# Kernel tuning notes

Hardware: AMD Instinct MI355X
Metric: run time of the kernel (lower is better)

## Reference

```python
import jax, jax.numpy as jnp
import numpy as np

B, N1, N2, D, H = 32, 512, 256, 256, 8
HD = D // H  # head dim = 32


def setup_inputs() -> dict:
    key = jax.random.key(0)
    ks = jax.random.split(key, 12)
    s = 0.05
    return {
        "x1": jax.random.normal(ks[0], (B, N1, D), jnp.float32),
        "x2": jax.random.normal(ks[1], (B, N2, D), jnp.float32),
        "r_w1": jax.random.normal(ks[2], (D, 2 * D), jnp.float32) * s,
        "r_b1": jnp.zeros((D,), jnp.float32),
        "ln_g": jnp.ones((D,), jnp.float32),
        "ln_b": jnp.zeros((D,), jnp.float32),
        "r_w2": jax.random.normal(ks[3], (4, D), jnp.float32) * s,
        "r_b2": jnp.zeros((4,), jnp.float32),
        "lf_w": jax.random.normal(ks[4], (D, D), jnp.float32) * s,
        "lf_b": jnp.zeros((D,), jnp.float32),
        "af2_w": jax.random.normal(ks[5], (D, D), jnp.float32) * s,
        "af2_b": jnp.zeros((D,), jnp.float32),
        "af3_w": jax.random.normal(ks[6], (N1, D), jnp.float32) * s,  # Linear(dim, num_pathway)
        "af3_b": jnp.zeros((N1,), jnp.float32),
        "attn_in_w": jax.random.normal(ks[7], (3 * D, D), jnp.float32) * s,
        "attn_in_b": jnp.zeros((3 * D,), jnp.float32),
        "attn_out_w": jax.random.normal(ks[8], (D, D), jnp.float32) * s,
        "attn_out_b": jnp.zeros((D,), jnp.float32),
    }


def _layernorm(x, g, b, eps=1e-5):
    mu = x.mean(-1, keepdims=True)
    var = ((x - mu) ** 2).mean(-1, keepdims=True)
    return (x - mu) * jax.lax.rsqrt(var + eps) * g + b


def reference(x1, x2, r_w1, r_b1, ln_g, ln_b, r_w2, r_b2,
              lf_w, lf_b, af2_w, af2_b, af3_w, af3_b,
              attn_in_w, attn_in_b, attn_out_w, attn_out_b):
    b, n1, d = x1.shape
    n2 = x2.shape[1]

    # ---- RoutingNetwork: mean-pool both modalities, small MLP, softmax ----
    m = jnp.concatenate([x1.mean(1), x2.mean(1)], axis=-1)        # [b, 2d]
    h = jax.nn.gelu(_layernorm(m @ r_w1.T + r_b1, ln_g, ln_b), approximate=False)
    logits = h @ r_w2.T + r_b2                                     # [b, 4]
    w = jax.nn.softmax(logits, axis=-1)                            # [b, 4]

    z = jnp.concatenate([x1, x2], axis=1)                          # [b, n1+n2, d]

    # ---- Expert 0: LinearFusion (dropout off at eval) ----
    lf = jax.nn.elu(z @ lf_w.T + lf_b)
    g0, i0 = lf[:, :n1, :], lf[:, n1:, :]

    # ---- Expert 1: AddFusion, n1 >= n2 branch (n2 == dim required) ----
    a1 = jax.nn.elu(x1 @ af2_w.T + af2_b)                          # [b, n1, d]
    a2 = jax.nn.elu(jnp.einsum('bnd,pn->bdp', x2, af3_w) + af3_b)  # [b, d, n1]
    a2 = a2.transpose(0, 2, 1)                                     # [b, n1, d]
    x_out = a1 + a2
    g1, i1 = x_out, x_out[:, :n2, :]

    # ---- Expert 2: AttentionFusion (MHA, 8 heads, self-attn over concat) ----
    qkv = z @ attn_in_w.T + attn_in_b                              # [b, S, 3d]
    q, k, v = jnp.split(qkv, 3, axis=-1)
    S = n1 + n2
    q = q.reshape(b, S, H, HD)
    k = k.reshape(b, S, H, HD)
    v = v.reshape(b, S, H, HD)
    scores = jnp.einsum('bqhd,bkhd->bhqk', q, k) / np.sqrt(HD)
    attn = jax.nn.softmax(scores, axis=-1)
    o = jnp.einsum('bhqk,bkhd->bqhd', attn, v).reshape(b, S, d)
    o = o @ attn_out_w.T + attn_out_b
    g2, i2 = o[:, :n1, :], o[:, n1:, :]

    # ---- Expert 3: IdentityFusion ----
    g3, i3 = x1, x2

    # ---- Soft-routing weighted combine ----
    gene_all = jnp.stack([g0, g1, g2, g3], axis=1)                 # [b, 4, n1, d]
    img_all = jnp.stack([i0, i1, i2, i3], axis=1)                  # [b, 4, n2, d]
    we = w[:, :, None, None]
    gene = (gene_all * we).sum(axis=1)
    img = (img_all * we).sum(axis=1)
    return gene, img
```

## Files before the change

### kernel.cpp

```cpp
#include <hip/hip_runtime.h>
#include <hip/hip_bf16.h>
#include <math.h>

#define B_ 32
#define N1_ 512
#define N2_ 256
#define D_ 256
#define S_ 768
#define IMG_OFF 4194304
#define QSCALE_ (0.17677669529663689f * 1.4426950408889634f)

typedef __attribute__((ext_vector_type(8))) short bf16x8;
typedef __attribute__((ext_vector_type(4))) float f32x4;
#define MFMA16(a, b, c) __builtin_amdgcn_mfma_f32_16x16x32_bf16(a, b, c, 0, 0, 0)

__device__ __forceinline__ ushort f2b(float f) {
  __hip_bfloat16 h = __float2bfloat16(f);
  return __builtin_bit_cast(ushort, h);
}
__device__ __forceinline__ uint pk2(float a, float b) {
  return (uint)f2b(a) | ((uint)f2b(b) << 16);
}
__device__ __forceinline__ float b2f(ushort u) {
  return __builtin_bit_cast(float, ((uint)u) << 16);
}
__device__ __forceinline__ float eluf(float v) { return v > 0.f ? v : expm1f(v); }

__device__ __forceinline__ void gl16(const ushort* g, ushort* l) {
  __builtin_amdgcn_global_load_lds(
      (const __attribute__((address_space(1))) uint*)g,
      (__attribute__((address_space(3))) uint*)l, 16, 0, 0);
}

__global__ __launch_bounds__(256) void k_prep(const float* __restrict__ x1,
                                              const float* __restrict__ x2,
                                              const float* __restrict__ lf_w,
                                              const float* __restrict__ af2_w,
                                              const float* __restrict__ af3_w,
                                              const float* __restrict__ attn_in_w,
                                              const float* __restrict__ attn_out_w,
                                              ushort* __restrict__ zb,
                                              ushort* __restrict__ wb,
                                              ushort* __restrict__ x2t,
                                              float* __restrict__ mp) {
  int t = threadIdx.x;
  if (blockIdx.x >= 256) {
    int g = (blockIdx.x - 256)*256 + t;
    int e0 = g*4;
    const float* src; int loc; float sc = 1.f;
    if (e0 < 65536)       { src = lf_w;       loc = e0; }
    else if (e0 < 131072) { src = af2_w;      loc = e0 - 65536; }
    else if (e0 < 262144) { src = af3_w;      loc = e0 - 131072; }
    else if (e0 < 458752) { src = attn_in_w;  loc = e0 - 262144; if (loc < 65536) sc = QSCALE_; }
    else                  { src = attn_out_w; loc = e0 - 458752; }
    float4 v = *(const float4*)(src + loc);
    *(ushort4*)(wb + e0) = make_ushort4(f2b(v.x*sc), f2b(v.y*sc), f2b(v.z*sc), f2b(v.w*sc));
    return;
  }
  int b = blockIdx.x >> 3, s = blockIdx.x & 7;
  int c = t & 63;
  int rg = t >> 6;
  __shared__ float red[4][260];
  __shared__ ushort xt[32][266];
  float4 s1 = {0.f, 0.f, 0.f, 0.f};
  for (int i = 0; i < 16; ++i) {
    int r = s*64 + rg*16 + i;
    float4 v = *(const float4*)(x1 + ((size_t)(b*N1_) + r)*D_ + c*4);
    s1.x += v.x; s1.y += v.y; s1.z += v.z; s1.w += v.w;
    uint2 pk; pk.x = pk2(v.x, v.y); pk.y = pk2(v.z, v.w);
    *(uint2*)(zb + (size_t)b*196608 + (size_t)r*256 + c*4) = pk;
  }
  red[rg][c*4+0] = s1.x; red[rg][c*4+1] = s1.y; red[rg][c*4+2] = s1.z; red[rg][c*4+3] = s1.w;
  __syncthreads();
  {
    float v = red[0][t] + red[1][t] + red[2][t] + red[3][t];
    mp[(size_t)(b*8+s)*512 + t] = v * (1.0f/512.0f);
  }
  __syncthreads();
  float4 s2 = {0.f, 0.f, 0.f, 0.f};
  for (int i = 0; i < 8; ++i) {
    int rl = rg*8 + i;
    int r = s*32 + rl;
    float4 v = *(const float4*)(x2 + ((size_t)(b*N2_) + r)*D_ + c*4);
    s2.x += v.x; s2.y += v.y; s2.z += v.z; s2.w += v.w;
    ushort b0 = f2b(v.x), b1 = f2b(v.y), b2 = f2b(v.z), b3 = f2b(v.w);
    uint2 pk; pk.x = (uint)b0 | ((uint)b1 << 16); pk.y = (uint)b2 | ((uint)b3 << 16);
    *(uint2*)(zb + (size_t)b*196608 + (size_t)(512 + r)*256 + c*4) = pk;
    xt[rl][c*4+0] = b0; xt[rl][c*4+1] = b1; xt[rl][c*4+2] = b2; xt[rl][c*4+3] = b3;
  }
  red[rg][c*4+0] = s2.x; red[rg][c*4+1] = s2.y; red[rg][c*4+2] = s2.z; red[rg][c*4+3] = s2.w;
  __syncthreads();
  {
    float v = red[0][t] + red[1][t] + red[2][t] + red[3][t];
    mp[(size_t)(b*8+s)*512 + 256 + t] = v * (1.0f/256.0f);
  }
  ushort* dst = x2t + (size_t)b*65536 + (size_t)t*256 + s*32;
  #pragma unroll
  for (int g = 0; g < 4; ++g) {
    uint4 w;
    w.x = (uint)xt[g*8+0][t] | ((uint)xt[g*8+1][t] << 16);
    w.y = (uint)xt[g*8+2][t] | ((uint)xt[g*8+3][t] << 16);
    w.z = (uint)xt[g*8+4][t] | ((uint)xt[g*8+5][t] << 16);
    w.w = (uint)xt[g*8+6][t] | ((uint)xt[g*8+7][t] << 16);
    *(uint4*)(dst + g*8) = w;
  }
}

__global__ __launch_bounds__(256) void k_head(const float* __restrict__ mp, const float* __restrict__ r_w1,
                       const float* __restrict__ r_b1, const float* __restrict__ ln_g,
                       const float* __restrict__ ln_b, const float* __restrict__ r_w2,
                       const float* __restrict__ r_b2, float* __restrict__ wout) {
  int b = blockIdx.x;
  int j = threadIdx.x;
  __shared__ __align__(16) float ms[512];
  __shared__ float red[256];
  float a0 = 0.f, a1 = 0.f;
  for (int s = 0; s < 8; ++s) {
    a0 += mp[(size_t)(b*8+s)*512 + j];
    a1 += mp[(size_t)(b*8+s)*512 + 256 + j];
  }
  ms[j] = a0; ms[j+256] = a1;
  __syncthreads();
  float4 accv = {0.f, 0.f, 0.f, 0.f};
  const float4* wrow4 = (const float4*)(r_w1 + (size_t)j*512);
  const float4* ms4 = (const float4*)ms;
  for (int k = 0; k < 128; ++k) {
    float4 w = wrow4[k], m = ms4[k];
    accv.x += w.x*m.x; accv.y += w.y*m.y; accv.z += w.z*m.z; accv.w += w.w*m.w;
  }
  float acc = r_b1[j] + (accv.x + accv.y) + (accv.z + accv.w);
  red[j] = acc; __syncthreads();
  for (int off=128; off>0; off>>=1){ if (j<off) red[j]+=red[j+off]; __syncthreads(); }
  float mu = red[0] * (1.f/256.f); __syncthreads();
  float cd = acc - mu;
  red[j] = cd*cd; __syncthreads();
  for (int off=128; off>0; off>>=1){ if (j<off) red[j]+=red[j+off]; __syncthreads(); }
  float var = red[0]*(1.f/256.f); __syncthreads();
  float xn = cd * rsqrtf(var + 1e-5f) * ln_g[j] + ln_b[j];
  float h = 0.5f*xn*(1.f+erff(xn*0.70710678118654752f));
  float lg[4];
  for (int e=0;e<4;++e){
    red[j] = h * r_w2[e*256 + j]; __syncthreads();
    for (int off=128; off>0; off>>=1){ if (j<off) red[j]+=red[j+off]; __syncthreads(); }
    lg[e] = red[0] + r_b2[e]; __syncthreads();
  }
  if (j==0){
    float mx = fmaxf(fmaxf(lg[0],lg[1]),fmaxf(lg[2],lg[3]));
    float e0=expf(lg[0]-mx),e1=expf(lg[1]-mx),e2=expf(lg[2]-mx),e3=expf(lg[3]-mx);
    float s=e0+e1+e2+e3;
    wout[b*4+0]=e0/s; wout[b*4+1]=e1/s; wout[b*4+2]=e2/s; wout[b*4+3]=e3/s;
  }
}

__global__ __launch_bounds__(256) void k_qkv(const ushort* __restrict__ zb, const ushort* __restrict__ wb,
                      const float* __restrict__ bias,
                      ushort* __restrict__ qo, ushort* __restrict__ kh,
                      ushort* __restrict__ vt) {
  int ct = blockIdx.x, nt = blockIdx.y, b = blockIdx.z;
  int tid = threadIdx.x;
  int lane = tid & 63, wid = tid >> 6;
  int wm = wid >> 1, wn = wid & 1;
  int l15 = lane & 15, quad = lane >> 4;
  __shared__ __align__(16) ushort As[128][64];
  __shared__ __align__(16) ushort Ws[128][64];
  f32x4 acc[4][4] = {};
  int n0 = nt*128, c0 = ct*128;
  const ushort* g_a = zb + (size_t)b*196608 + (size_t)(n0 + wid*32 + (lane>>3))*256 + (lane&7)*8;
  const ushort* g_w = wb + 262144 + (size_t)(c0 + wid*32 + (lane>>3))*256 + (lane&7)*8;
  for (int k0 = 0; k0 < 256; k0 += 64) {
    #pragma unroll
    for (int j = 0; j < 4; ++j) {
      gl16(g_a + (size_t)j*8*256 + k0, &As[wid*32 + j*8][0]);
      gl16(g_w + (size_t)j*8*256 + k0, &Ws[wid*32 + j*8][0]);
    }
    __syncthreads();
    #pragma unroll
    for (int kc = 0; kc < 2; ++kc) {
      bf16x8 af[4], bfr[4];
      #pragma unroll
      for (int im = 0; im < 4; ++im) af[im] = *(bf16x8*)&As[wm*64 + im*16 + l15][kc*32 + quad*8];
      #pragma unroll
      for (int in = 0; in < 4; ++in) bfr[in] = *(bf16x8*)&Ws[wn*64 + in*16 + l15][kc*32 + quad*8];
      #pragma unroll
      for (int im = 0; im < 4; ++im)
        #pragma unroll
        for (int in = 0; in < 4; ++in)
          acc[im][in] = MFMA16(af[im], bfr[in], acc[im][in]);
    }
    __syncthreads();
  }
  if (ct < 2) {
    #pragma unroll
    for (int im = 0; im < 4; ++im)
      #pragma unroll
      for (int reg = 0; reg < 4; ++reg) {
        int n = n0 + wm*64 + im*16 + quad*4 + reg;
        #pragma unroll
        for (int in = 0; in < 4; ++in) {
          int c = c0 + wn*64 + in*16 + l15;
          qo[((size_t)(b*S_)+n)*256 + c] = f2b(acc[im][in][reg] + bias[c]*QSCALE_);
        }
      }
  } else if (ct < 4) {
    #pragma unroll
    for (int im = 0; im < 4; ++im)
      #pragma unroll
      for (int reg = 0; reg < 4; ++reg) {
        int n = n0 + wm*64 + im*16 + quad*4 + reg;
        #pragma unroll
        for (int in = 0; in < 4; ++in) {
          int c = c0 + wn*64 + in*16 + l15;
          int kc2 = c - 256; int h = kc2 >> 5, d = kc2 & 31;
          kh[(((size_t)(b*8+h))*S_ + n)*32 + d] = f2b(acc[im][in][reg] + bias[c]);
        }
      }
  } else {
    #pragma unroll
    for (int im = 0; im < 4; ++im) {
      int nb = n0 + wm*64 + im*16 + quad*4;
      #pragma unroll
      for (int in = 0; in < 4; ++in) {
        int c = c0 + wn*64 + in*16 + l15;
        float bs = bias[c];
        int vcol = c - 512; int h = vcol >> 5, d = vcol & 31;
        uint2 pk;
        pk.x = pk2(acc[im][in][0] + bs, acc[im][in][1] + bs);
        pk.y = pk2(acc[im][in][2] + bs, acc[im][in][3] + bs);
        *(uint2*)&vt[(((size_t)(b*8+h))*32 + d)*S_ + nb] = pk;
      }
    }
  }
}

__global__ __launch_bounds__(256) void k_attn(const ushort* __restrict__ qo,
                                              const ushort* __restrict__ kh,
                                              const ushort* __restrict__ vt,
                                              ushort* __restrict__ obuf) {
  int qhf = blockIdx.x, h = blockIdx.y, b = blockIdx.z;
  int tid = threadIdx.x;
  int lane = tid & 63, w = tid >> 6;
  int l15 = lane & 15, quad = lane >> 4;
  __shared__ __align__(16) ushort Ks[64][32];
  __shared__ __align__(16) ushort Vts[32][64];
  __shared__ __align__(16) ushort Ps[4][16][72];

  int qbase = qhf*384 + w*96;
  bf16x8 bq[6];
  #pragma unroll
  for (int u = 0; u < 6; ++u)
    bq[u] = *(const bf16x8*)(qo + ((size_t)(b*S_) + qbase + u*16 + l15)*256 + h*32 + quad*8);

  f32x4 ao[6][2] = {};
  float lacc[6] = {};

  const ushort* khb = kh + ((size_t)(b*8+h))*S_*32;
  const ushort* vtb = vt + ((size_t)(b*8+h))*32*S_;
  const ushort* g_k = khb + (size_t)(w*16 + (lane>>2))*32 + (lane&3)*8;
  const ushort* g_v = vtb + (size_t)(w*8 + (lane>>3))*S_ + (lane&7)*8;

  for (int kt = 0; kt < 12; ++kt) {
    __syncthreads();
    gl16(g_k + (size_t)(kt*64)*32, &Ks[w*16][0]);
    gl16(g_v + kt*64, &Vts[w*8][0]);
    __syncthreads();

    bf16x8 ak[4];
    #pragma unroll
    for (int t = 0; t < 4; ++t) ak[t] = *(bf16x8*)&Ks[t*16 + l15][quad*8];
    bf16x8 av[2][2];
    #pragma unroll
    for (int im = 0; im < 2; ++im)
      #pragma unroll
      for (int kc = 0; kc < 2; ++kc)
        av[im][kc] = *(bf16x8*)&Vts[im*16 + l15][kc*32 + quad*8];

    #pragma unroll
    for (int u = 0; u < 6; ++u) {
      f32x4 sf[4];
      #pragma unroll
      for (int t = 0; t < 4; ++t) {
        f32x4 z = {0.f, 0.f, 0.f, 0.f};
        sf[t] = MFMA16(ak[t], bq[u], z);
      }
      #pragma unroll
      for (int t = 0; t < 4; ++t) {
        float p0 = __builtin_amdgcn_exp2f(sf[t][0]);
        float p1 = __builtin_amdgcn_exp2f(sf[t][1]);
        float p2 = __builtin_amdgcn_exp2f(sf[t][2]);
        float p3 = __builtin_amdgcn_exp2f(sf[t][3]);
        lacc[u] += (p0 + p1) + (p2 + p3);
        uint2 pk;
        pk.x = pk2(p0, p1);
        pk.y = pk2(p2, p3);
        *(uint2*)&Ps[w][l15][t*16 + quad*4] = pk;
      }
      #pragma unroll
      for (int kc = 0; kc < 2; ++kc) {
        bf16x8 bp = *(bf16x8*)&Ps[w][l15][kc*32 + quad*8];
        ao[u][0] = MFMA16(av[0][kc], bp, ao[u][0]);
        ao[u][1] = MFMA16(av[1][kc], bp, ao[u][1]);
      }
    }
  }
  #pragma unroll
  for (int u = 0; u < 6; ++u) {
    float l = lacc[u];
    l += __shfl_xor(l, 16, 64);
    l += __shfl_xor(l, 32, 64);
    float linv = 1.f / l;
    int n = qbase + u*16 + l15;
    ushort* orow = obuf + ((size_t)(b*S_)+n)*256 + h*32;
    #pragma unroll
    for (int im = 0; im < 2; ++im) {
      uint2 pk;
      pk.x = pk2(ao[u][im][0]*linv, ao[u][im][1]*linv);
      pk.y = pk2(ao[u][im][2]*linv, ao[u][im][3]*linv);
      *(uint2*)(orow + im*16 + quad*4) = pk;
    }
  }
}

__global__ __launch_bounds__(256) void k_out(const ushort* __restrict__ zb, const ushort* __restrict__ wb,
                      const ushort* __restrict__ ob, const ushort* __restrict__ x2t,
                      const float* __restrict__ lf_b, const float* __restrict__ af2_b,
                      const float* __restrict__ af3_b, const float* __restrict__ ao_b,
                      const float* __restrict__ wgt, float* __restrict__ out) {
  int dt = blockIdx.x, nt = blockIdx.y, b = blockIdx.z;
  int tid = threadIdx.x;
  int lane = tid & 63, wid = tid >> 6;
  int wm = wid >> 1, wn = wid & 1;
  int l15 = lane & 15, quad = lane >> 4;
  __shared__ __align__(16) ushort A1[64][32];
  __shared__ __align__(16) ushort A2[64][32];
  __shared__ __align__(16) ushort A3[64][32];
  __shared__ __align__(16) ushort A4[64][32];
  __shared__ __align__(16) ushort W1s[64][32];
  __shared__ __align__(16) ushort W2s[64][32];
  __shared__ __align__(16) ushort W3s[64][32];
  __shared__ __align__(16) ushort W4s[64][32];
  f32x4 a_lf[2][2] = {}, a_a1[2][2] = {}, a_a2[2][2] = {}, a_pj[2][2] = {};
  int n0 = nt*64, d0 = dt*64;
  int xr0 = ((nt < 8) ? nt : (nt - 8)) * 64;
  int sr = tid >> 2, sc4 = (tid & 3) * 8;

  const ushort* p_a1 = zb + (size_t)b*196608 + (size_t)(n0+sr)*256 + sc4;
  const ushort* p_a2 = zb + (size_t)b*196608 + (size_t)(xr0+sr)*256 + sc4;
  const ushort* p_a3 = wb + 131072 + (size_t)(xr0+sr)*256 + sc4;
  const ushort* p_a4 = ob + ((size_t)(b*S_) + n0 + sr)*256 + sc4;
  const ushort* p_w1 = wb + (size_t)(d0+sr)*256 + sc4;
  const ushort* p_w2 = wb + 65536 + (size_t)(d0+sr)*256 + sc4;
  const ushort* p_w3 = x2t + (size_t)b*65536 + (size_t)(d0+sr)*256 + sc4;
  const ushort* p_w4 = wb + 458752 + (size_t)(d0+sr)*256 + sc4;
  ushort* l_a1 = &A1[wid*16][0];
  ushort* l_a2 = &A2[wid*16][0];
  ushort* l_a3 = &A3[wid*16][0];
  ushort* l_a4 = &A4[wid*16][0];
  ushort* l_w1 = &W1s[wid*16][0];
  ushort* l_w2 = &W2s[wid*16][0];
  ushort* l_w3 = &W3s[wid*16][0];
  ushort* l_w4 = &W4s[wid*16][0];

  for (int k0 = 0; k0 < 256; k0 += 32) {
    gl16(p_a1 + k0, l_a1);
    gl16(p_a2 + k0, l_a2);
    gl16(p_a3 + k0, l_a3);
    gl16(p_a4 + k0, l_a4);
    gl16(p_w1 + k0, l_w1);
    gl16(p_w2 + k0, l_w2);
    gl16(p_w3 + k0, l_w3);
    gl16(p_w4 + k0, l_w4);
    __syncthreads();
    {
      int ko = quad*8;
      bf16x8 x0, x1r, y0, y1;
      x0 = *(bf16x8*)&A1[wm*32 + l15][ko];  x1r = *(bf16x8*)&A1[wm*32 + 16 + l15][ko];
      y0 = *(bf16x8*)&W1s[wn*32 + l15][ko]; y1  = *(bf16x8*)&W1s[wn*32 + 16 + l15][ko];
      a_lf[0][0] = MFMA16(x0, y0, a_lf[0][0]);  a_lf[0][1] = MFMA16(x0, y1, a_lf[0][1]);
      a_lf[1][0] = MFMA16(x1r, y0, a_lf[1][0]); a_lf[1][1] = MFMA16(x1r, y1, a_lf[1][1]);
      x0 = *(bf16x8*)&A2[wm*32 + l15][ko];  x1r = *(bf16x8*)&A2[wm*32 + 16 + l15][ko];
      y0 = *(bf16x8*)&W2s[wn*32 + l15][ko]; y1  = *(bf16x8*)&W2s[wn*32 + 16 + l15][ko];
      a_a1[0][0] = MFMA16(x0, y0, a_a1[0][0]);  a_a1[0][1] = MFMA16(x0, y1, a_a1[0][1]);
      a_a1[1][0] = MFMA16(x1r, y0, a_a1[1][0]); a_a1[1][1] = MFMA16(x1r, y1, a_a1[1][1]);
      x0 = *(bf16x8*)&A3[wm*32 + l15][ko];  x1r = *(bf16x8*)&A3[wm*32 + 16 + l15][ko];
      y0 = *(bf16x8*)&W3s[wn*32 + l15][ko]; y1  = *(bf16x8*)&W3s[wn*32 + 16 + l15][ko];
      a_a2[0][0] = MFMA16(x0, y0, a_a2[0][0]);  a_a2[0][1] = MFMA16(x0, y1, a_a2[0][1]);
      a_a2[1][0] = MFMA16(x1r, y0, a_a2[1][0]); a_a2[1][1] = MFMA16(x1r, y1, a_a2[1][1]);
      x0 = *(bf16x8*)&A4[wm*32 + l15][ko];  x1r = *(bf16x8*)&A4[wm*32 + 16 + l15][ko];
      y0 = *(bf16x8*)&W4s[wn*32 + l15][ko]; y1  = *(bf16x8*)&W4s[wn*32 + 16 + l15][ko];
      a_pj[0][0] = MFMA16(x0, y0, a_pj[0][0]);  a_pj[0][1] = MFMA16(x0, y1, a_pj[0][1]);
      a_pj[1][0] = MFMA16(x1r, y0, a_pj[1][0]); a_pj[1][1] = MFMA16(x1r, y1, a_pj[1][1]);
    }
    __syncthreads();
  }
  float w0 = wgt[b*4+0], w1v = wgt[b*4+1], w2v = wgt[b*4+2], w3 = wgt[b*4+3];
  #pragma unroll
  for (int im = 0; im < 2; ++im) {
    #pragma unroll
    for (int reg = 0; reg < 4; ++reg) {
      int rl = wm*32 + im*16 + quad*4 + reg;
      int n = n0 + rl;
      int rx = xr0 + rl;
      const ushort* zr = zb + (size_t)b*196608 + (size_t)n*256;
      float* orw = (nt < 8) ? out + ((size_t)(b*N1_) + n)*D_
                            : out + (size_t)IMG_OFF + ((size_t)(b*N2_) + (n - 512))*D_;
      float b3 = af3_b[rx];
      #pragma unroll
      for (int in = 0; in < 2; ++in) {
        int d = d0 + wn*32 + in*16 + l15;
        float v = w0*eluf(a_lf[im][in][reg] + lf_b[d])
                + w1v*(eluf(a_a1[im][in][reg] + af2_b[d]) + eluf(a_a2[im][in][reg] + b3))
                + w2v*(a_pj[im][in][reg] + ao_b[d])
                + w3*b2f(zr[d]);
        orw[d] = v;
      }
    }
  }
}

extern "C" void kernel_launch(void* const* d_in, const int* in_sizes, int n_in,
                              void* d_out, int out_size, void* d_ws, size_t ws_size,
                              hipStream_t stream) {
  const float* x1        = (const float*)d_in[0];
  const float* x2        = (const float*)d_in[1];
  const float* r_w1      = (const float*)d_in[2];
  const float* r_b1      = (const float*)d_in[3];
  const float* ln_g      = (const float*)d_in[4];
  const float* ln_b      = (const float*)d_in[5];
  const float* r_w2      = (const float*)d_in[6];
  const float* r_b2      = (const float*)d_in[7];
  const float* lf_b      = (const float*)d_in[9];
  const float* af2_b     = (const float*)d_in[11];
  const float* af3_b     = (const float*)d_in[13];
  const float* attn_in_b = (const float*)d_in[15];
  const float* attn_out_b= (const float*)d_in[17];
  float* out = (float*)d_out;

  float* ws_mp = (float*)d_ws;
  float* ws_w  = ws_mp + 131072;
  ushort* ws_zb = (ushort*)(ws_w + 128);
  ushort* ws_qo = ws_zb + (size_t)B_*S_*256;
  ushort* ws_kh = ws_qo + (size_t)B_*S_*256;
  ushort* ws_vt = ws_kh + (size_t)B_*S_*256;
  ushort* ws_wb = ws_vt + (size_t)B_*S_*256;
  ushort* ws_xt = ws_wb + 524288;

  k_prep<<<dim3(768), 256, 0, stream>>>(x1, x2, (const float*)d_in[8], (const float*)d_in[10],
                                        (const float*)d_in[12], (const float*)d_in[14],
                                        (const float*)d_in[16], ws_zb, ws_wb, ws_xt, ws_mp);
  k_head<<<dim3(B_),   256, 0, stream>>>(ws_mp, r_w1, r_b1, ln_g, ln_b, r_w2, r_b2, ws_w);
  k_qkv <<<dim3(6,6,B_), 256, 0, stream>>>(ws_zb, ws_wb, attn_in_b, ws_qo, ws_kh, ws_vt);
  k_attn<<<dim3(2,8,B_), 256, 0, stream>>>(ws_qo, ws_kh, ws_vt, ws_qo);
  k_out <<<dim3(4,12,B_),256, 0, stream>>>(ws_zb, ws_wb, ws_qo, ws_xt,
                                           lf_b, af2_b, af3_b, attn_out_b, ws_w, out);
}
```

Before: 250.1 us.

## XOR-swizzle LDS tiles in GEMM and attention kernels, split attention finer

Applies an XOR swizzle to the shared-memory layout of the QKV GEMM, the attention K/V tiles and the fused output GEMM. Global-to-LDS writes and MFMA fragment reads are permuted so that 16-byte accesses spread across banks and avoid LDS bank conflicts. The output kernel also packs pairs of 32-wide operand tiles into 64-wide tiles. The attention grid doubles its query splitting (4 blocks of 192 rows instead of 2 of 384) and reorders grid dimensions. This gives more blocks and fewer registers per thread for occupancy, at the cost of reloading K/V more often.

```diff
diff --git a/kernel.cpp b/kernel.cpp
--- a/kernel.cpp
+++ b/kernel.cpp
@@ -165,8 +165,10 @@
   __shared__ __align__(16) ushort Ws[128][64];
   f32x4 acc[4][4] = {};
   int n0 = nt*128, c0 = ct*128;
-  const ushort* g_a = zb + (size_t)b*196608 + (size_t)(n0 + wid*32 + (lane>>3))*256 + (lane&7)*8;
-  const ushort* g_w = wb + 262144 + (size_t)(c0 + wid*32 + (lane>>3))*256 + (lane&7)*8;
+  int rl8 = lane >> 3, ss = (lane & 7) ^ rl8;
+  const ushort* g_a = zb + (size_t)b*196608 + (size_t)(n0 + wid*32 + rl8)*256 + ss*8;
+  const ushort* g_w = wb + 262144 + (size_t)(c0 + wid*32 + rl8)*256 + ss*8;
+  int l7 = l15 & 7;
   for (int k0 = 0; k0 < 256; k0 += 64) {
     #pragma unroll
     for (int j = 0; j < 4; ++j) {
@@ -176,11 +178,12 @@
     __syncthreads();
     #pragma unroll
     for (int kc = 0; kc < 2; ++kc) {
+      int cpx = ((kc*4 + quad) ^ l7) * 8;
       bf16x8 af[4], bfr[4];
       #pragma unroll
-      for (int im = 0; im < 4; ++im) af[im] = *(bf16x8*)&As[wm*64 + im*16 + l15][kc*32 + quad*8];
-      #pragma unroll
-      for (int in = 0; in < 4; ++in) bfr[in] = *(bf16x8*)&Ws[wn*64 + in*16 + l15][kc*32 + quad*8];
+      for (int im = 0; im < 4; ++im) af[im] = *(bf16x8*)&As[wm*64 + im*16 + l15][cpx];
+      #pragma unroll
+      for (int in = 0; in < 4; ++in) bfr[in] = *(bf16x8*)&Ws[wn*64 + in*16 + l15][cpx];
       #pragma unroll
       for (int im = 0; im < 4; ++im)
         #pragma unroll
@@ -236,46 +239,50 @@
                                               const ushort* __restrict__ kh,
                                               const ushort* __restrict__ vt,
                                               ushort* __restrict__ obuf) {
-  int qhf = blockIdx.x, h = blockIdx.y, b = blockIdx.z;
+  int h = blockIdx.x, b = blockIdx.y, qhf = blockIdx.z;
   int tid = threadIdx.x;
   int lane = tid & 63, w = tid >> 6;
   int l15 = lane & 15, quad = lane >> 4;
-  __shared__ __align__(16) ushort Ks[64][32];
+  __shared__ __align__(16) ushort Ks2[32][64];
   __shared__ __align__(16) ushort Vts[32][64];
   __shared__ __align__(16) ushort Ps[4][16][72];
 
-  int qbase = qhf*384 + w*96;
-  bf16x8 bq[6];
+  int qbase = qhf*192 + w*48;
+  bf16x8 bq[3];
   #pragma unroll
-  for (int u = 0; u < 6; ++u)
+  for (int u = 0; u < 3; ++u)
     bq[u] = *(const bf16x8*)(qo + ((size_t)(b*S_) + qbase + u*16 + l15)*256 + h*32 + quad*8);
 
-  f32x4 ao[6][2] = {};
-  float lacc[6] = {};
+  f32x4 ao[3][2] = {};
+  float lacc[3] = {};
 
   const ushort* khb = kh + ((size_t)(b*8+h))*S_*32;
   const ushort* vtb = vt + ((size_t)(b*8+h))*32*S_;
-  const ushort* g_k = khb + (size_t)(w*16 + (lane>>2))*32 + (lane&3)*8;
-  const ushort* g_v = vtb + (size_t)(w*8 + (lane>>3))*S_ + (lane&7)*8;
+  int rl8 = lane >> 3, ss = (lane & 7) ^ rl8;
+  const ushort* g_k = khb + (size_t)(2*(w*8 + rl8) + (ss >> 2))*32 + (ss & 3)*8;
+  const ushort* g_v = vtb + (size_t)(w*8 + rl8)*S_ + ss*8;
+
+  int cpk = (((l15 & 1)*4 + quad) ^ ((l15 >> 1) & 7)) * 8;
+  int l7 = l15 & 7;
 
   for (int kt = 0; kt < 12; ++kt) {
     __syncthreads();
-    gl16(g_k + (size_t)(kt*64)*32, &Ks[w*16][0]);
+    gl16(g_k + (size_t)kt*64*32, &Ks2[w*8][0]);
     gl16(g_v + kt*64, &Vts[w*8][0]);
     __syncthreads();
 
     bf16x8 ak[4];
     #pragma unroll
-    for (int t = 0; t < 4; ++t) ak[t] = *(bf16x8*)&Ks[t*16 + l15][quad*8];
+    for (int t = 0; t < 4; ++t) ak[t] = *(bf16x8*)&Ks2[t*8 + (l15 >> 1)][cpk];
     bf16x8 av[2][2];
     #pragma unroll
     for (int im = 0; im < 2; ++im)
       #pragma unroll
       for (int kc = 0; kc < 2; ++kc)
-        av[im][kc] = *(bf16x8*)&Vts[im*16 + l15][kc*32 + quad*8];
-
-    #pragma unroll
-    for (int u = 0; u < 6; ++u) {
+        av[im][kc] = *(bf16x8*)&Vts[im*16 + l15][((kc*4 + quad) ^ l7) * 8];
+
+    #pragma unroll
+    for (int u = 0; u < 3; ++u) {
       f32x4 sf[4];
       #pragma unroll
       for (int t = 0; t < 4; ++t) {
@@ -303,7 +310,7 @@
     }
   }
   #pragma unroll
-  for (int u = 0; u < 6; ++u) {
+  for (int u = 0; u < 3; ++u) {
     float l = lacc[u];
     l += __shfl_xor(l, 16, 64);
     l += __shfl_xor(l, 32, 64);
@@ -330,63 +337,56 @@
   int lane = tid & 63, wid = tid >> 6;
   int wm = wid >> 1, wn = wid & 1;
   int l15 = lane & 15, quad = lane >> 4;
-  __shared__ __align__(16) ushort A1[64][32];
-  __shared__ __align__(16) ushort A2[64][32];
-  __shared__ __align__(16) ushort A3[64][32];
-  __shared__ __align__(16) ushort A4[64][32];
-  __shared__ __align__(16) ushort W1s[64][32];
-  __shared__ __align__(16) ushort W2s[64][32];
-  __shared__ __align__(16) ushort W3s[64][32];
-  __shared__ __align__(16) ushort W4s[64][32];
+  __shared__ __align__(16) ushort PAB[64][64];
+  __shared__ __align__(16) ushort PCD[64][64];
+  __shared__ __align__(16) ushort PWX[64][64];
+  __shared__ __align__(16) ushort PYZ[64][64];
   f32x4 a_lf[2][2] = {}, a_a1[2][2] = {}, a_a2[2][2] = {}, a_pj[2][2] = {};
   int n0 = nt*64, d0 = dt*64;
   int xr0 = ((nt < 8) ? nt : (nt - 8)) * 64;
-  int sr = tid >> 2, sc4 = (tid & 3) * 8;
-
-  const ushort* p_a1 = zb + (size_t)b*196608 + (size_t)(n0+sr)*256 + sc4;
-  const ushort* p_a2 = zb + (size_t)b*196608 + (size_t)(xr0+sr)*256 + sc4;
-  const ushort* p_a3 = wb + 131072 + (size_t)(xr0+sr)*256 + sc4;
-  const ushort* p_a4 = ob + ((size_t)(b*S_) + n0 + sr)*256 + sc4;
-  const ushort* p_w1 = wb + (size_t)(d0+sr)*256 + sc4;
-  const ushort* p_w2 = wb + 65536 + (size_t)(d0+sr)*256 + sc4;
-  const ushort* p_w3 = x2t + (size_t)b*65536 + (size_t)(d0+sr)*256 + sc4;
-  const ushort* p_w4 = wb + 458752 + (size_t)(d0+sr)*256 + sc4;
-  ushort* l_a1 = &A1[wid*16][0];
-  ushort* l_a2 = &A2[wid*16][0];
-  ushort* l_a3 = &A3[wid*16][0];
-  ushort* l_a4 = &A4[wid*16][0];
-  ushort* l_w1 = &W1s[wid*16][0];
-  ushort* l_w2 = &W2s[wid*16][0];
-  ushort* l_w3 = &W3s[wid*16][0];
-  ushort* l_w4 = &W4s[wid*16][0];
+
+  int rl8 = lane >> 3, ss = (lane & 7) ^ rl8;
+  int sel2 = ss >> 2;
+  int km = (ss & 3) * 8;
+  int r_st = wid*16 + rl8;
+  const ushort* pAB = (sel2 ? zb + (size_t)b*196608 + (size_t)(xr0+r_st)*256
+                            : zb + (size_t)b*196608 + (size_t)(n0+r_st)*256) + km;
+  const ushort* pCD = (sel2 ? ob + ((size_t)(b*S_) + n0 + r_st)*256
+                            : wb + 131072 + (size_t)(xr0+r_st)*256) + km;
+  const ushort* pWX = (sel2 ? wb + 65536 + (size_t)(d0+r_st)*256
+                            : wb + (size_t)(d0+r_st)*256) + km;
+  const ushort* pYZ = (sel2 ? wb + 458752 + (size_t)(d0+r_st)*256
+                            : x2t + (size_t)b*65536 + (size_t)(d0+r_st)*256) + km;
+
+  int l7 = l15 & 7;
+  int c1 = (quad ^ l7) * 8;
+  int c2 = ((quad + 4) ^ l7) * 8;
 
   for (int k0 = 0; k0 < 256; k0 += 32) {
-    gl16(p_a1 + k0, l_a1);
-    gl16(p_a2 + k0, l_a2);
-    gl16(p_a3 + k0, l_a3);
-    gl16(p_a4 + k0, l_a4);
-    gl16(p_w1 + k0, l_w1);
-    gl16(p_w2 + k0, l_w2);
-    gl16(p_w3 + k0, l_w3);
-    gl16(p_w4 + k0, l_w4);
+    #pragma unroll
+    for (int j = 0; j < 2; ++j) {
+      gl16(pAB + k0 + j*2048, &PAB[wid*16 + j*8][0]);
+      gl16(pCD + k0 + j*2048, &PCD[wid*16 + j*8][0]);
+      gl16(pWX + k0 + j*2048, &PWX[wid*16 + j*8][0]);
+      gl16(pYZ + k0 + j*2048, &PYZ[wid*16 + j*8][0]);
+    }
     __syncthreads();
     {
-      int ko = quad*8;
       bf16x8 x0, x1r, y0, y1;
-      x0 = *(bf16x8*)&A1[wm*32 + l15][ko];  x1r = *(bf16x8*)&A1[wm*32 + 16 + l15][ko];
-      y0 = *(bf16x8*)&W1s[wn*32 + l15][ko]; y1  = *(bf16x8*)&W1s[wn*32 + 16 + l15][ko];
+      x0 = *(bf16x8*)&PAB[wm*32 + l15][c1];  x1r = *(bf16x8*)&PAB[wm*32 + 16 + l15][c1];
+      y0 = *(bf16x8*)&PWX[wn*32 + l15][c1];  y1  = *(bf16x8*)&PWX[wn*32 + 16 + l15][c1];
       a_lf[0][0] = MFMA16(x0, y0, a_lf[0][0]);  a_lf[0][1] = MFMA16(x0, y1, a_lf[0][1]);
       a_lf[1][0] = MFMA16(x1r, y0, a_lf[1][0]); a_lf[1][1] = MFMA16(x1r, y1, a_lf[1][1]);
-      x0 = *(bf16x8*)&A2[wm*32 + l15][ko];  x1r = *(bf16x8*)&A2[wm*32 + 16 + l15][ko];
-      y0 = *(bf16x8*)&W2s[wn*32 + l15][ko]; y1  = *(bf16x8*)&W2s[wn*32 + 16 + l15][ko];
+      x0 = *(bf16x8*)&PAB[wm*32 + l15][c2];  x1r = *(bf16x8*)&PAB[wm*32 + 16 + l15][c2];
+      y0 = *(bf16x8*)&PWX[wn*32 + l15][c2];  y1  = *(bf16x8*)&PWX[wn*32 + 16 + l15][c2];
       a_a1[0][0] = MFMA16(x0, y0, a_a1[0][0]);  a_a1[0][1] = MFMA16(x0, y1, a_a1[0][1]);
       a_a1[1][0] = MFMA16(x1r, y0, a_a1[1][0]); a_a1[1][1] = MFMA16(x1r, y1, a_a1[1][1]);
-      x0 = *(bf16x8*)&A3[wm*32 + l15][ko];  x1r = *(bf16x8*)&A3[wm*32 + 16 + l15][ko];
-      y0 = *(bf16x8*)&W3s[wn*32 + l15][ko]; y1  = *(bf16x8*)&W3s[wn*32 + 16 + l15][ko];
+      x0 = *(bf16x8*)&PCD[wm*32 + l15][c1];  x1r = *(bf16x8*)&PCD[wm*32 + 16 + l15][c1];
+      y0 = *(bf16x8*)&PYZ[wn*32 + l15][c1];  y1  = *(bf16x8*)&PYZ[wn*32 + 16 + l15][c1];
       a_a2[0][0] = MFMA16(x0, y0, a_a2[0][0]);  a_a2[0][1] = MFMA16(x0, y1, a_a2[0][1]);
       a_a2[1][0] = MFMA16(x1r, y0, a_a2[1][0]); a_a2[1][1] = MFMA16(x1r, y1, a_a2[1][1]);
-      x0 = *(bf16x8*)&A4[wm*32 + l15][ko];  x1r = *(bf16x8*)&A4[wm*32 + 16 + l15][ko];
-      y0 = *(bf16x8*)&W4s[wn*32 + l15][ko]; y1  = *(bf16x8*)&W4s[wn*32 + 16 + l15][ko];
+      x0 = *(bf16x8*)&PCD[wm*32 + l15][c2];  x1r = *(bf16x8*)&PCD[wm*32 + 16 + l15][c2];
+      y0 = *(bf16x8*)&PYZ[wn*32 + l15][c2];  y1  = *(bf16x8*)&PYZ[wn*32 + 16 + l15][c2];
       a_pj[0][0] = MFMA16(x0, y0, a_pj[0][0]);  a_pj[0][1] = MFMA16(x0, y1, a_pj[0][1]);
       a_pj[1][0] = MFMA16(x1r, y0, a_pj[1][0]); a_pj[1][1] = MFMA16(x1r, y1, a_pj[1][1]);
     }
@@ -449,7 +449,7 @@
                                         (const float*)d_in[16], ws_zb, ws_wb, ws_xt, ws_mp);
   k_head<<<dim3(B_),   256, 0, stream>>>(ws_mp, r_w1, r_b1, ln_g, ln_b, r_w2, r_b2, ws_w);
   k_qkv <<<dim3(6,6,B_), 256, 0, stream>>>(ws_zb, ws_wb, attn_in_b, ws_qo, ws_kh, ws_vt);
-  k_attn<<<dim3(2,8,B_), 256, 0, stream>>>(ws_qo, ws_kh, ws_vt, ws_qo);
+  k_attn<<<dim3(8,B_,4), 256, 0, stream>>>(ws_qo, ws_kh, ws_vt, ws_qo);
   k_out <<<dim3(4,12,B_),256, 0, stream>>>(ws_zb, ws_wb, ws_qo, ws_xt,
                                            lf_b, af2_b, af3_b, attn_out_b, ws_w, out);
 }
```

New measurement: 251.2 us. About the same (+0.4%).

## XOR-swizzle LDS tiles to avoid bank conflicts and split attention queries finer

Applied to the files above, without the earlier changes.

Applies an XOR swizzle to the shared-memory staging of the A/W tiles in the QKV and output GEMMs and to the K/V tiles in attention, so the 16-byte fragment reads hit distinct LDS banks. The attention kernel also halves the queries per block (from 384 to 192), doubling the grid to 1024 blocks and reordering grid dimensions. This is meant to cut LDS bank conflicts and raise occupancy in attention. The cost is redundant K/V tile loads across more blocks.

```diff
diff --git a/kernel.cpp b/kernel.cpp
--- a/kernel.cpp
+++ b/kernel.cpp
@@ -165,8 +165,10 @@
   __shared__ __align__(16) ushort Ws[128][64];
   f32x4 acc[4][4] = {};
   int n0 = nt*128, c0 = ct*128;
-  const ushort* g_a = zb + (size_t)b*196608 + (size_t)(n0 + wid*32 + (lane>>3))*256 + (lane&7)*8;
-  const ushort* g_w = wb + 262144 + (size_t)(c0 + wid*32 + (lane>>3))*256 + (lane&7)*8;
+  int rl8 = lane >> 3, ss = (lane & 7) ^ rl8;
+  const ushort* g_a = zb + (size_t)b*196608 + (size_t)(n0 + wid*32 + rl8)*256 + ss*8;
+  const ushort* g_w = wb + 262144 + (size_t)(c0 + wid*32 + rl8)*256 + ss*8;
+  int l7 = l15 & 7;
   for (int k0 = 0; k0 < 256; k0 += 64) {
     #pragma unroll
     for (int j = 0; j < 4; ++j) {
@@ -176,11 +178,12 @@
     __syncthreads();
     #pragma unroll
     for (int kc = 0; kc < 2; ++kc) {
+      int cpx = ((kc*4 + quad) ^ l7) * 8;
       bf16x8 af[4], bfr[4];
       #pragma unroll
-      for (int im = 0; im < 4; ++im) af[im] = *(bf16x8*)&As[wm*64 + im*16 + l15][kc*32 + quad*8];
-      #pragma unroll
-      for (int in = 0; in < 4; ++in) bfr[in] = *(bf16x8*)&Ws[wn*64 + in*16 + l15][kc*32 + quad*8];
+      for (int im = 0; im < 4; ++im) af[im] = *(bf16x8*)&As[wm*64 + im*16 + l15][cpx];
+      #pragma unroll
+      for (int in = 0; in < 4; ++in) bfr[in] = *(bf16x8*)&Ws[wn*64 + in*16 + l15][cpx];
       #pragma unroll
       for (int im = 0; im < 4; ++im)
         #pragma unroll
@@ -236,46 +239,50 @@
                                               const ushort* __restrict__ kh,
                                               const ushort* __restrict__ vt,
                                               ushort* __restrict__ obuf) {
-  int qhf = blockIdx.x, h = blockIdx.y, b = blockIdx.z;
+  int h = blockIdx.x, b = blockIdx.y, qhf = blockIdx.z;
   int tid = threadIdx.x;
   int lane = tid & 63, w = tid >> 6;
   int l15 = lane & 15, quad = lane >> 4;
-  __shared__ __align__(16) ushort Ks[64][32];
+  __shared__ __align__(16) ushort Ks2[32][64];
   __shared__ __align__(16) ushort Vts[32][64];
   __shared__ __align__(16) ushort Ps[4][16][72];
 
-  int qbase = qhf*384 + w*96;
-  bf16x8 bq[6];
+  int qbase = qhf*192 + w*48;
+  bf16x8 bq[3];
   #pragma unroll
-  for (int u = 0; u < 6; ++u)
+  for (int u = 0; u < 3; ++u)
     bq[u] = *(const bf16x8*)(qo + ((size_t)(b*S_) + qbase + u*16 + l15)*256 + h*32 + quad*8);
 
-  f32x4 ao[6][2] = {};
-  float lacc[6] = {};
+  f32x4 ao[3][2] = {};
+  float lacc[3] = {};
 
   const ushort* khb = kh + ((size_t)(b*8+h))*S_*32;
   const ushort* vtb = vt + ((size_t)(b*8+h))*32*S_;
-  const ushort* g_k = khb + (size_t)(w*16 + (lane>>2))*32 + (lane&3)*8;
-  const ushort* g_v = vtb + (size_t)(w*8 + (lane>>3))*S_ + (lane&7)*8;
+  int rl8 = lane >> 3, ss = (lane & 7) ^ rl8;
+  const ushort* g_k = khb + (size_t)(2*(w*8 + rl8) + (ss >> 2))*32 + (ss & 3)*8;
+  const ushort* g_v = vtb + (size_t)(w*8 + rl8)*S_ + ss*8;
+
+  int cpk = (((l15 & 1)*4 + quad) ^ ((l15 >> 1) & 7)) * 8;
+  int l7 = l15 & 7;
 
   for (int kt = 0; kt < 12; ++kt) {
     __syncthreads();
-    gl16(g_k + (size_t)(kt*64)*32, &Ks[w*16][0]);
+    gl16(g_k + (size_t)kt*64*32, &Ks2[w*8][0]);
     gl16(g_v + kt*64, &Vts[w*8][0]);
     __syncthreads();
 
     bf16x8 ak[4];
     #pragma unroll
-    for (int t = 0; t < 4; ++t) ak[t] = *(bf16x8*)&Ks[t*16 + l15][quad*8];
+    for (int t = 0; t < 4; ++t) ak[t] = *(bf16x8*)&Ks2[t*8 + (l15 >> 1)][cpk];
     bf16x8 av[2][2];
     #pragma unroll
     for (int im = 0; im < 2; ++im)
       #pragma unroll
       for (int kc = 0; kc < 2; ++kc)
-        av[im][kc] = *(bf16x8*)&Vts[im*16 + l15][kc*32 + quad*8];
-
-    #pragma unroll
-    for (int u = 0; u < 6; ++u) {
+        av[im][kc] = *(bf16x8*)&Vts[im*16 + l15][((kc*4 + quad) ^ l7) * 8];
+
+    #pragma unroll
+    for (int u = 0; u < 3; ++u) {
       f32x4 sf[4];
       #pragma unroll
       for (int t = 0; t < 4; ++t) {
@@ -303,7 +310,7 @@
     }
   }
   #pragma unroll
-  for (int u = 0; u < 6; ++u) {
+  for (int u = 0; u < 3; ++u) {
     float l = lacc[u];
     l += __shfl_xor(l, 16, 64);
     l += __shfl_xor(l, 32, 64);
@@ -341,7 +348,8 @@
   f32x4 a_lf[2][2] = {}, a_a1[2][2] = {}, a_a2[2][2] = {}, a_pj[2][2] = {};
   int n0 = nt*64, d0 = dt*64;
   int xr0 = ((nt < 8) ? nt : (nt - 8)) * 64;
-  int sr = tid >> 2, sc4 = (tid & 3) * 8;
+  int sr = tid >> 2;
+  int sc4 = (((lane & 3) ^ ((lane >> 3) & 3))) * 8;
 
   const ushort* p_a1 = zb + (size_t)b*196608 + (size_t)(n0+sr)*256 + sc4;
   const ushort* p_a2 = zb + (size_t)b*196608 + (size_t)(xr0+sr)*256 + sc4;
@@ -360,6 +368,8 @@
   ushort* l_w3 = &W3s[wid*16][0];
   ushort* l_w4 = &W4s[wid*16][0];
 
+  int cq = (quad ^ ((l15 >> 1) & 3)) * 8;
+
   for (int k0 = 0; k0 < 256; k0 += 32) {
     gl16(p_a1 + k0, l_a1);
     gl16(p_a2 + k0, l_a2);
@@ -371,22 +381,21 @@
     gl16(p_w4 + k0, l_w4);
     __syncthreads();
     {
-      int ko = quad*8;
       bf16x8 x0, x1r, y0, y1;
-      x0 = *(bf16x8*)&A1[wm*32 + l15][ko];  x1r = *(bf16x8*)&A1[wm*32 + 16 + l15][ko];
-      y0 = *(bf16x8*)&W1s[wn*32 + l15][ko]; y1  = *(bf16x8*)&W1s[wn*32 + 16 + l15][ko];
+      x0 = *(bf16x8*)&A1[wm*32 + l15][cq];  x1r = *(bf16x8*)&A1[wm*32 + 16 + l15][cq];
+      y0 = *(bf16x8*)&W1s[wn*32 + l15][cq]; y1  = *(bf16x8*)&W1s[wn*32 + 16 + l15][cq];
       a_lf[0][0] = MFMA16(x0, y0, a_lf[0][0]);  a_lf[0][1] = MFMA16(x0, y1, a_lf[0][1]);
       a_lf[1][0] = MFMA16(x1r, y0, a_lf[1][0]); a_lf[1][1] = MFMA16(x1r, y1, a_lf[1][1]);
-      x0 = *(bf16x8*)&A2[wm*32 + l15][ko];  x1r = *(bf16x8*)&A2[wm*32 + 16 + l15][ko];
-      y0 = *(bf16x8*)&W2s[wn*32 + l15][ko]; y1  = *(bf16x8*)&W2s[wn*32 + 16 + l15][ko];
+      x0 = *(bf16x8*)&A2[wm*32 + l15][cq];  x1r = *(bf16x8*)&A2[wm*32 + 16 + l15][cq];
+      y0 = *(bf16x8*)&W2s[wn*32 + l15][cq]; y1  = *(bf16x8*)&W2s[wn*32 + 16 + l15][cq];
       a_a1[0][0] = MFMA16(x0, y0, a_a1[0][0]);  a_a1[0][1] = MFMA16(x0, y1, a_a1[0][1]);
       a_a1[1][0] = MFMA16(x1r, y0, a_a1[1][0]); a_a1[1][1] = MFMA16(x1r, y1, a_a1[1][1]);
-      x0 = *(bf16x8*)&A3[wm*32 + l15][ko];  x1r = *(bf16x8*)&A3[wm*32 + 16 + l15][ko];
-      y0 = *(bf16x8*)&W3s[wn*32 + l15][ko]; y1  = *(bf16x8*)&W3s[wn*32 + 16 + l15][ko];
+      x0 = *(bf16x8*)&A3[wm*32 + l15][cq];  x1r = *(bf16x8*)&A3[wm*32 + 16 + l15][cq];
+      y0 = *(bf16x8*)&W3s[wn*32 + l15][cq]; y1  = *(bf16x8*)&W3s[wn*32 + 16 + l15][cq];
       a_a2[0][0] = MFMA16(x0, y0, a_a2[0][0]);  a_a2[0][1] = MFMA16(x0, y1, a_a2[0][1]);
       a_a2[1][0] = MFMA16(x1r, y0, a_a2[1][0]); a_a2[1][1] = MFMA16(x1r, y1, a_a2[1][1]);
-      x0 = *(bf16x8*)&A4[wm*32 + l15][ko];  x1r = *(bf16x8*)&A4[wm*32 + 16 + l15][ko];
-      y0 = *(bf16x8*)&W4s[wn*32 + l15][ko]; y1  = *(bf16x8*)&W4s[wn*32 + 16 + l15][ko];
+      x0 = *(bf16x8*)&A4[wm*32 + l15][cq];  x1r = *(bf16x8*)&A4[wm*32 + 16 + l15][cq];
+      y0 = *(bf16x8*)&W4s[wn*32 + l15][cq]; y1  = *(bf16x8*)&W4s[wn*32 + 16 + l15][cq];
       a_pj[0][0] = MFMA16(x0, y0, a_pj[0][0]);  a_pj[0][1] = MFMA16(x0, y1, a_pj[0][1]);
       a_pj[1][0] = MFMA16(x1r, y0, a_pj[1][0]); a_pj[1][1] = MFMA16(x1r, y1, a_pj[1][1]);
     }
@@ -449,7 +458,7 @@
                                         (const float*)d_in[16], ws_zb, ws_wb, ws_xt, ws_mp);
   k_head<<<dim3(B_),   256, 0, stream>>>(ws_mp, r_w1, r_b1, ln_g, ln_b, r_w2, r_b2, ws_w);
   k_qkv <<<dim3(6,6,B_), 256, 0, stream>>>(ws_zb, ws_wb, attn_in_b, ws_qo, ws_kh, ws_vt);
-  k_attn<<<dim3(2,8,B_), 256, 0, stream>>>(ws_qo, ws_kh, ws_vt, ws_qo);
+  k_attn<<<dim3(8,B_,4), 256, 0, stream>>>(ws_qo, ws_kh, ws_vt, ws_qo);
   k_out <<<dim3(4,12,B_),256, 0, stream>>>(ws_zb, ws_wb, ws_qo, ws_xt,
                                            lf_b, af2_b, af3_b, attn_out_b, ws_w, out);
 }
```

After: 242.2 us. -3.2%, faster.
